# Kernel tuning notes

Hardware: AMD Instinct MI355X
Metric: run time of the kernel (lower is better)

## Reference

```python
import jax, jax.numpy as jnp
import numpy as np

B, S, H, N = 2, 2048, 1024, 16
D = H // N


def setup_inputs() -> dict:
    key = jax.random.key(0)
    k1, k2, k3 = jax.random.split(key, 3)
    # Xavier-uniform-ish init for projection weights
    lim_in = (6.0 / (H + 3 * H)) ** 0.5
    lim_out = (6.0 / (H + H)) ** 0.5
    return {
        "hidden_states": jax.random.normal(k1, (B, S, H), dtype=jnp.float32),
        "w_in": jax.random.uniform(k2, (3 * H, H), minval=-lim_in, maxval=lim_in, dtype=jnp.float32),
        "b_in": jnp.zeros((3 * H,), dtype=jnp.float32),
        "w_out": jax.random.uniform(k3, (H, H), minval=-lim_out, maxval=lim_out, dtype=jnp.float32),
        "b_out": jnp.zeros((H,), dtype=jnp.float32),
    }


def reference(hidden_states, w_in, b_in, w_out, b_out):
    b, s, h = hidden_states.shape
    qkv = hidden_states @ w_in.T + b_in  # [B,S,3H]
    q, k, v = jnp.split(qkv, 3, axis=-1)
    # [B,S,H] -> [B,N,S,D]
    def to_heads(x):
        return x.reshape(b, s, N, D).transpose(0, 2, 1, 3)
    q, k, v = to_heads(q), to_heads(k), to_heads(v)
    scale = D ** -0.5
    scores = jnp.einsum("bnqd,bnkd->bnqk", q, k) * scale  # [B,N,S,S]
    causal = jnp.triu(jnp.ones((s, s), dtype=bool), k=1)
    scores = jnp.where(causal, -jnp.inf, scores)
    attn = jax.nn.softmax(scores, axis=-1)
    out = jnp.einsum("bnqk,bnkd->bnqd", attn, v)  # [B,N,S,D]
    out = out.transpose(0, 2, 1, 3).reshape(b, s, h)
    return out @ w_out.T + b_out
```

## Files before the change

### kernel.cpp

```cpp
#include <hip/hip_runtime.h>
#include <hip/hip_bf16.h>

#define BB 2
#define SS 2048
#define HH 1024
#define NH 16
#define DD 64
#define H3 3072
#define MM (BB*SS)

typedef unsigned short u16;
typedef unsigned int u32;
typedef __attribute__((ext_vector_type(8))) short bf16x8;
typedef __attribute__((ext_vector_type(4))) float f32x4;

__device__ __forceinline__ u16 f2bf(float f) {
    union { float f; u32 u; } v; v.f = f;
    u32 u = v.u;
    u += 0x7fffu + ((u >> 16) & 1u);
    return (u16)(u >> 16);
}
__device__ __forceinline__ float bf2f(u16 h) {
    union { u32 u; float f; } v; v.u = ((u32)h) << 16;
    return v.f;
}
__device__ __forceinline__ u32 pack2bf(float a, float b) {
    __hip_bfloat162 h = __float22bfloat162_rn(float2{a, b});
    u32 u; __builtin_memcpy(&u, &h, 4);
    return u;
}
__device__ __forceinline__ float exp2v(float x) {
    float r;
    asm volatile("v_exp_f32 %0, %1" : "=v"(r) : "v"(x));
    return r;
}
__device__ __forceinline__ void gl_lds16(const void* g, void* l) {
    __builtin_amdgcn_global_load_lds(
        (const __attribute__((address_space(1))) u32*)g,
        (__attribute__((address_space(3))) u32*)l, 16, 0, 0);
}
__device__ __forceinline__ int ginv(int R) {
    return (R & 35) | ((R & 8) << 1) | ((R & 4) << 1) | ((R & 16) >> 2);
}

__global__ void cvt3bf(const float4* __restrict__ s0, uint2* __restrict__ d0, int n0,
                       const float4* __restrict__ s1, uint2* __restrict__ d1, int n1,
                       const float4* __restrict__ s2, uint2* __restrict__ d2, int n2) {
    int i = blockIdx.x * blockDim.x + threadIdx.x;
    const int tot = n0 + n1 + n2;
    for (; i < tot; i += gridDim.x * blockDim.x) {
        const float4* s; uint2* d; int j;
        if (i < n0)            { s = s0; d = d0; j = i; }
        else if (i < n0 + n1)  { s = s1; d = d1; j = i - n0; }
        else                   { s = s2; d = d2; j = i - n0 - n1; }
        float4 v = s[j];
        uint2 o; o.x = pack2bf(v.x, v.y); o.y = pack2bf(v.z, v.w);
        d[j] = o;
    }
}

template<int BN, int MODE>
__global__ __launch_bounds__(256, 3)
void gemm_k2(const u16* __restrict__ A, const u16* __restrict__ Bbf,
             const u16* __restrict__ biasbf, void* __restrict__ Cptr,
             u16* __restrict__ Qo, u16* __restrict__ Ko, u16* __restrict__ Vto,
             int M, int Nn, int K)
{
    constexpr int NFR = BN / 32;
    __shared__ __align__(16) u16 Alds[2][128 * 32];
    __shared__ __align__(16) u16 Blds[2][BN * 32];
    const int tid = threadIdx.x;
    const int w = tid >> 6, lane = tid & 63, quad = lane >> 4, l16 = lane & 15;
    const int gx = gridDim.x, nwg = gx * gridDim.y;
    const int f = blockIdx.y * gx + blockIdx.x;
    const int wg = (f & 7) * (nwg >> 3) + (f >> 3);
    const int m0 = (wg % gx) * 128, n0 = (wg / gx) * BN;
    const int wm = w >> 1, wn = w & 1;
    const int rA4 = lane >> 2, c8b = (lane & 3) * 8;

    f32x4 acc[4][NFR] = {};

#define GSTAGE(k0_, bi_) do {                                                  \
    _Pragma("unroll")                                                          \
    for (int q = 0; q < 2; ++q) {                                              \
        int row0 = w * 32 + q * 16;                                            \
        gl_lds16(&A[(size_t)(m0 + row0 + rA4) * K + (k0_) + c8b],              \
                 &Alds[bi_][row0 * 32]);                                       \
    }                                                                          \
    _Pragma("unroll")                                                          \
    for (int q = 0; q < BN / 64; ++q) {                                        \
        int row0 = w * (BN / 4) + q * 16;                                      \
        gl_lds16(&Bbf[(size_t)(n0 + row0 + rA4) * K + (k0_) + c8b],            \
                 &Blds[bi_][row0 * 32]);                                       \
    }                                                                          \
} while (0)

    const int NT = K >> 5;
    GSTAGE(0, 0);
    for (int t = 0; t < NT; ++t) {
        const int cur = t & 1;
        __syncthreads();
        if (t + 1 < NT) GSTAGE((t + 1) << 5, cur ^ 1);

        bf16x8 af[4], bfr[NFR];
#pragma unroll
        for (int mi = 0; mi < 4; ++mi)
            af[mi] = *(const bf16x8*)&Alds[cur][(wm * 64 + mi * 16 + l16) * 32 + quad * 8];
#pragma unroll
        for (int ni = 0; ni < NFR; ++ni)
            bfr[ni] = *(const bf16x8*)&Blds[cur][(wn * (BN / 2) + ni * 16 + l16) * 32 + quad * 8];
#pragma unroll
        for (int mi = 0; mi < 4; ++mi)
#pragma unroll
            for (int ni = 0; ni < NFR; ++ni)
                acc[mi][ni] = __builtin_amdgcn_mfma_f32_16x16x32_bf16(
                    af[mi], bfr[ni], acc[mi][ni], 0, 0, 0);
    }
#undef GSTAGE

#pragma unroll
    for (int mi = 0; mi < 4; ++mi) {
        int row_b = m0 + wm * 64 + mi * 16 + quad * 4;
#pragma unroll
        for (int ni = 0; ni < NFR; ++ni) {
            int col = n0 + wn * (BN / 2) + ni * 16 + l16;
            float bv = bf2f(biasbf[col]);
            if constexpr (MODE == 1) {
#pragma unroll
                for (int i = 0; i < 4; ++i)
                    ((float*)Cptr)[(size_t)(row_b + i) * Nn + col] = acc[mi][ni][i] + bv;
            } else {
                if (col < 1024) {
#pragma unroll
                    for (int i = 0; i < 4; ++i)
                        Qo[(size_t)(row_b + i) * 1024 + col] =
                            f2bf((acc[mi][ni][i] + bv) * 0.18033688f);
                } else if (col < 2048) {
#pragma unroll
                    for (int i = 0; i < 4; ++i)
                        Ko[(size_t)(row_b + i) * 1024 + (col - 1024)] =
                            f2bf(acc[mi][ni][i] + bv);
                } else {
                    int d = col - 2048, hh = d >> 6, dd = d & 63;
                    int b = row_b >> 11, s = row_b & 2047;
                    u16 t0 = f2bf(acc[mi][ni][0] + bv), t1 = f2bf(acc[mi][ni][1] + bv);
                    u16 t2 = f2bf(acc[mi][ni][2] + bv), t3 = f2bf(acc[mi][ni][3] + bv);
                    uint2 pk; pk.x = (u32)t0 | ((u32)t1 << 16);
                    pk.y = (u32)t2 | ((u32)t3 << 16);
                    *(uint2*)&Vto[((size_t)((b * 16 + hh) * 64 + dd)) * 2048 + s] = pk;
                }
            }
        }
    }
}

__global__ __launch_bounds__(256, 2)
void attn_v10(const u16* __restrict__ Q, const u16* __restrict__ Kb,
              const u16* __restrict__ Vt, u16* __restrict__ attn_out) {
    const int bid = blockIdx.x;
    const int r8 = bid & 7, qq = bid >> 3;
    const int pr = qq >> 2, g = (qq & 3) * 8 + r8;
    const int h = g & 15, b = g >> 4;
    const int tid = threadIdx.x;
    const int w = tid >> 6, lane = tid & 63, quad = lane >> 4, l16 = lane & 15;
    __shared__ __align__(16) u16 Klds[2][64 * 64];
    __shared__ __align__(16) u16 Vlds[2][64 * 64];

    const int sl = lane >> 3, cch = lane & 7;
    const int rho0 = (2 * w) * 8 + sl, rho1 = (2 * w + 1) * 8 + sl;
    const int gcs = (cch ^ sl) * 8;
    const int kg0 = ginv(rho0), kg1 = ginv(rho1);
    const int ls0 = (2 * w) * 512, ls1 = (2 * w + 1) * 512;
    const int xk0 = (quad ^ (l16 & 7)) * 8;
    const int xk1 = ((quad + 4) ^ (l16 & 7)) * 8;

    for (int half = 0; half < 2; ++half) {
        const int qt = half ? pr : (31 - pr);
        const int q0 = qt * 64;
        const int T = qt + 1;

        const u16* Qb = Q  + (size_t)(b * SS + q0) * 1024 + h * 64;
        const u16* Kg = Kb + (size_t)(b * SS) * 1024 + h * 64;
        const u16* Vg = Vt + (size_t)((b * 16 + h) * 64) * 2048;

#define STAGE_T(kv0_, bi_) do {                                               \
        gl_lds16(&Kg[(size_t)((kv0_) + kg0) * 1024 + gcs], &Klds[bi_][ls0]);  \
        gl_lds16(&Kg[(size_t)((kv0_) + kg1) * 1024 + gcs], &Klds[bi_][ls1]);  \
        gl_lds16(&Vg[(size_t)rho0 * 2048 + (kv0_) + gcs], &Vlds[bi_][ls0]);   \
        gl_lds16(&Vg[(size_t)rho1 * 2048 + (kv0_) + gcs], &Vlds[bi_][ls1]);   \
    } while (0)

        bf16x8 qf0 = *(const bf16x8*)&Qb[(size_t)(w * 16 + l16) * 1024 + quad * 8];
        bf16x8 qf1 = *(const bf16x8*)&Qb[(size_t)(w * 16 + l16) * 1024 + 32 + quad * 8];

        f32x4 oacc[4] = {};
        float lp = 0.f;

        __syncthreads();
        STAGE_T(0, 0);

        for (int t = 0; t < T; ++t) {
            const int cur = t & 1;
            __syncthreads();
            if (t + 1 < T) STAGE_T((t + 1) * 64, cur ^ 1);
            const u16* Kc = Klds[cur];
            const u16* Vc = Vlds[cur];
            f32x4 sacc[4] = {};
#pragma unroll
            for (int ni = 0; ni < 4; ++ni) {
                const int rb = (ni * 16 + l16) * 64;
                bf16x8 kf0 = *(const bf16x8*)&Kc[rb + xk0];
                bf16x8 kf1 = *(const bf16x8*)&Kc[rb + xk1];
                sacc[ni] = __builtin_amdgcn_mfma_f32_16x16x32_bf16(kf0, qf0, sacc[ni], 0, 0, 0);
                sacc[ni] = __builtin_amdgcn_mfma_f32_16x16x32_bf16(kf1, qf1, sacc[ni], 0, 0, 0);
            }
            u32 pk[4][2];
            if (t + 1 < T) {
#pragma unroll
                for (int ni = 0; ni < 4; ++ni) {
                    float p0 = exp2v(sacc[ni][0]), p1 = exp2v(sacc[ni][1]);
                    float p2 = exp2v(sacc[ni][2]), p3 = exp2v(sacc[ni][3]);
                    lp += (p0 + p1) + (p2 + p3);
                    pk[ni][0] = pack2bf(p0, p1);
                    pk[ni][1] = pack2bf(p2, p3);
                }
            } else {
                const int thr = w * 16 + l16;
#pragma unroll
                for (int ni = 0; ni < 4; ++ni) {
                    const int pb = 32 * (ni >> 1) + 8 * quad + 4 * (ni & 1);
                    float pv[4];
#pragma unroll
                    for (int i = 0; i < 4; ++i) {
                        float e = exp2v(sacc[ni][i]);
                        pv[i] = (pb + i <= thr) ? e : 0.f;
                    }
                    lp += (pv[0] + pv[1]) + (pv[2] + pv[3]);
                    pk[ni][0] = pack2bf(pv[0], pv[1]);
                    pk[ni][1] = pack2bf(pv[2], pv[3]);
                }
            }
            union { u32 u[4]; bf16x8 v; } pf0, pf1;
            pf0.u[0] = pk[0][0]; pf0.u[1] = pk[0][1];
            pf0.u[2] = pk[1][0]; pf0.u[3] = pk[1][1];
            pf1.u[0] = pk[2][0]; pf1.u[1] = pk[2][1];
            pf1.u[2] = pk[3][0]; pf1.u[3] = pk[3][1];
#pragma unroll
            for (int ni = 0; ni < 4; ++ni) {
                const int rb = (ni * 16 + l16) * 64;
                bf16x8 vf0 = *(const bf16x8*)&Vc[rb + xk0];
                bf16x8 vf1 = *(const bf16x8*)&Vc[rb + xk1];
                oacc[ni] = __builtin_amdgcn_mfma_f32_16x16x32_bf16(pf0.v, vf0, oacc[ni], 0, 0, 0);
                oacc[ni] = __builtin_amdgcn_mfma_f32_16x16x32_bf16(pf1.v, vf1, oacc[ni], 0, 0, 0);
            }
        }

        lp += __shfl_xor(lp, 16, 64);
        lp += __shfl_xor(lp, 32, 64);
        float linv[4];
#pragma unroll
        for (int i = 0; i < 4; ++i)
            linv[i] = 1.0f / __shfl(lp, quad * 4 + i, 64);

        u16* ob = attn_out + (size_t)(b * SS + q0 + w * 16) * 1024 + h * 64;
#pragma unroll
        for (int ni = 0; ni < 4; ++ni)
#pragma unroll
            for (int i = 0; i < 4; ++i)
                ob[(size_t)(quad * 4 + i) * 1024 + ni * 16 + l16] =
                    f2bf(oacc[ni][i] * linv[i]);
#undef STAGE_T
    }
}

extern "C" void kernel_launch(void* const* d_in, const int* in_sizes, int n_in,
                              void* d_out, int out_size, void* d_ws, size_t ws_size,
                              hipStream_t stream) {
    const float* hidden = (const float*)d_in[0];
    const float* w_in   = (const float*)d_in[1];
    const float* b_in   = (const float*)d_in[2];
    const float* w_out  = (const float*)d_in[3];
    const float* b_out  = (const float*)d_in[4];
    float* out = (float*)d_out;

    char* ws = (char*)d_ws;
    u16* hid_bf  = (u16*)d_out;
    u16* wi_bf   = (u16*)ws;
    u16* bi_bf   = (u16*)(ws + 6291456);
    u16* attn_ws = (u16*)ws;
    u16* Qbuf    = (u16*)(ws + 8388608);
    u16* wo_bf   = (u16*)(ws + 8388608);
    u16* bo_bf   = (u16*)(ws + 8388608 + 2097152);
    u16* Kbuf    = (u16*)(ws + 16777216);
    u16* Vtbuf   = (u16*)(ws + 25165824);

    cvt3bf<<<dim3(2048), dim3(256), 0, stream>>>(
        (const float4*)hidden, (uint2*)hid_bf, 1048576,
        (const float4*)w_in,   (uint2*)wi_bf,  786432,
        (const float4*)b_in,   (uint2*)bi_bf,  768);
    gemm_k2<128, 2><<<dim3(32, 24), dim3(256), 0, stream>>>(
        hid_bf, wi_bf, bi_bf, nullptr, Qbuf, Kbuf, Vtbuf, MM, H3, HH);
    attn_v10<<<dim3(512), dim3(256), 0, stream>>>(
        Qbuf, Kbuf, Vtbuf, attn_ws);
    cvt3bf<<<dim3(512), dim3(256), 0, stream>>>(
        (const float4*)w_out, (uint2*)wo_bf, 262144,
        (const float4*)b_out, (uint2*)bo_bf, 256,
        nullptr, nullptr, 0);
    gemm_k2<64, 1><<<dim3(32, 16), dim3(256), 0, stream>>>(
        attn_ws, wo_bf, bo_bf, out, nullptr, nullptr, nullptr, MM, HH, HH);
}
```

Before: 176.4 us.

## Replace QKV projection GEMM with 256x256-tile 8-wave pipelined kernel

Swaps the 128x128-tile QKV GEMM for a new 512-thread kernel that computes 256x256 output tiles. It uses a 128 KB LDS double buffer with XOR-swizzled layout and direct global-to-LDS loads, interleaved with MFMA quarter-phases through explicit vmcnt waits, barriers and setprio. The larger tiles raise data reuse, and the fine-grained staging aims to hide load latency behind MFMA work. In exchange the grid shrinks to 192 blocks, so fewer workgroups are in flight. The hand-tuned wait counts are fragile and must exactly match the number of outstanding loads.

```diff
diff --git a/kernel.cpp b/kernel.cpp
--- a/kernel.cpp
+++ b/kernel.cpp
@@ -42,6 +42,8 @@
 __device__ __forceinline__ int ginv(int R) {
     return (R & 35) | ((R & 8) << 1) | ((R & 4) << 1) | ((R & 16) >> 2);
 }
+
+#define VMW(N) asm volatile("s_waitcnt vmcnt(" #N ")" ::: "memory")
 
 __global__ void cvt3bf(const float4* __restrict__ s0, uint2* __restrict__ d0, int n0,
                        const float4* __restrict__ s1, uint2* __restrict__ d1, int n1,
@@ -56,6 +58,126 @@
         float4 v = s[j];
         uint2 o; o.x = pack2bf(v.x, v.y); o.y = pack2bf(v.z, v.w);
         d[j] = o;
+    }
+}
+
+__global__ __launch_bounds__(512, 2)
+void gemm8_qkv(const u16* __restrict__ Aw, const u16* __restrict__ Bw,
+               const u16* __restrict__ biasbf,
+               u16* __restrict__ Qo, u16* __restrict__ Ko, u16* __restrict__ Vto)
+{
+    __shared__ __align__(16) u16 L[65536];
+    const int tid = threadIdx.x;
+    const int w = tid >> 6, lane = tid & 63, quad = lane >> 4, l16 = lane & 15;
+    const int wm = w >> 2, wn = w & 3;
+    const int f = blockIdx.x;
+    const int wgs = (f & 7) * 24 + (f >> 3);
+    const int m0 = (wgs & 15) * 256, n0 = (wgs >> 4) * 256;
+    const int rl8 = lane >> 3;
+    const int gcs = ((lane & 7) ^ rl8) * 8;
+    const int xk0 = (quad ^ (l16 & 7)) * 8;
+    const int xk1 = ((quad + 4) ^ (l16 & 7)) * 8;
+
+    f32x4 acc[8][4] = {};
+
+#define STAGE8(ISB, H_, BUF, KT) do {                                          \
+    const u16* gsrc_ = (ISB) ? Bw : Aw;                                        \
+    const int gr0_ = ((ISB) ? n0 : m0) + (H_) * 128;                           \
+    _Pragma("unroll")                                                          \
+    for (int j = 0; j < 2; ++j) {                                              \
+        int s_ = 2 * w + j;                                                    \
+        gl_lds16(&gsrc_[(size_t)(gr0_ + s_ * 8 + rl8) * 1024 + (KT) * 64 + gcs], \
+                 &L[((BUF) * 4 + (ISB) * 2 + (H_)) * 8192 + s_ * 512]);        \
+    }                                                                          \
+} while (0)
+
+#define PH(MH, NH, CBUF, STG, WT) do {                                         \
+    bf16x8 afr[4][2], bfr2[2][2];                                              \
+    const u16* Ab_ = &L[((CBUF) * 4 + (MH)) * 8192];                           \
+    const u16* Bb_ = &L[((CBUF) * 4 + 2 + (NH)) * 8192];                       \
+    _Pragma("unroll")                                                          \
+    for (int m4 = 0; m4 < 4; ++m4) {                                           \
+        int r_ = (((((MH) * 4 + m4) * 2 + wm) & 7) << 4) + l16;                \
+        afr[m4][0] = *(const bf16x8*)&Ab_[r_ * 64 + xk0];                      \
+        afr[m4][1] = *(const bf16x8*)&Ab_[r_ * 64 + xk1];                      \
+    }                                                                          \
+    _Pragma("unroll")                                                          \
+    for (int n2 = 0; n2 < 2; ++n2) {                                           \
+        int rb_ = (((((NH) * 2 + n2) * 4 + wn) & 7) << 4) + l16;               \
+        bfr2[n2][0] = *(const bf16x8*)&Bb_[rb_ * 64 + xk0];                    \
+        bfr2[n2][1] = *(const bf16x8*)&Bb_[rb_ * 64 + xk1];                    \
+    }                                                                          \
+    STG;                                                                       \
+    __builtin_amdgcn_s_barrier();                                              \
+    __builtin_amdgcn_s_setprio(1);                                             \
+    _Pragma("unroll")                                                          \
+    for (int m4 = 0; m4 < 4; ++m4)                                             \
+        _Pragma("unroll")                                                      \
+        for (int n2 = 0; n2 < 2; ++n2) {                                       \
+            acc[(MH)*4+m4][(NH)*2+n2] = __builtin_amdgcn_mfma_f32_16x16x32_bf16( \
+                afr[m4][0], bfr2[n2][0], acc[(MH)*4+m4][(NH)*2+n2], 0, 0, 0);  \
+            acc[(MH)*4+m4][(NH)*2+n2] = __builtin_amdgcn_mfma_f32_16x16x32_bf16( \
+                afr[m4][1], bfr2[n2][1], acc[(MH)*4+m4][(NH)*2+n2], 0, 0, 0);  \
+        }                                                                      \
+    __builtin_amdgcn_s_setprio(0);                                             \
+    WT;                                                                        \
+    __builtin_amdgcn_s_barrier();                                              \
+} while (0)
+
+    STAGE8(0, 0, 0, 0); STAGE8(1, 0, 0, 0);
+    STAGE8(0, 1, 0, 0); STAGE8(1, 1, 0, 0);
+    STAGE8(0, 0, 1, 1); STAGE8(1, 0, 1, 1);
+    VMW(8);
+    __builtin_amdgcn_s_barrier();
+
+    for (int it = 0; it < 7; ++it) {
+        PH(0, 0, 0, STAGE8(0, 1, 1, 2 * it + 1), VMW(6));
+        PH(0, 1, 0, STAGE8(1, 1, 1, 2 * it + 1), VMW(10));
+        PH(1, 0, 0, STAGE8(0, 0, 0, 2 * it + 2), ((void)0));
+        PH(1, 1, 0, STAGE8(1, 0, 0, 2 * it + 2), VMW(8));
+        PH(0, 0, 1, STAGE8(0, 1, 0, 2 * it + 2), VMW(6));
+        PH(0, 1, 1, STAGE8(1, 1, 0, 2 * it + 2), VMW(10));
+        PH(1, 0, 1, STAGE8(0, 0, 1, 2 * it + 3), ((void)0));
+        PH(1, 1, 1, STAGE8(1, 0, 1, 2 * it + 3), VMW(8));
+    }
+    PH(0, 0, 0, STAGE8(0, 1, 1, 15), VMW(6));
+    PH(0, 1, 0, STAGE8(1, 1, 1, 15), VMW(10));
+    PH(1, 0, 0, ((void)0), ((void)0));
+    PH(1, 1, 0, ((void)0), VMW(4));
+    PH(0, 0, 1, ((void)0), VMW(0));
+    PH(0, 1, 1, ((void)0), ((void)0));
+    PH(1, 0, 1, ((void)0), ((void)0));
+    PH(1, 1, 1, ((void)0), ((void)0));
+#undef PH
+#undef STAGE8
+
+#pragma unroll
+    for (int mi = 0; mi < 8; ++mi) {
+        int row_b = m0 + (2 * mi + wm) * 16 + quad * 4;
+#pragma unroll
+        for (int ni = 0; ni < 4; ++ni) {
+            int col = n0 + (4 * ni + wn) * 16 + l16;
+            float bv = bf2f(biasbf[col]);
+            if (col < 1024) {
+#pragma unroll
+                for (int i = 0; i < 4; ++i)
+                    Qo[(size_t)(row_b + i) * 1024 + col] =
+                        f2bf((acc[mi][ni][i] + bv) * 0.18033688f);
+            } else if (col < 2048) {
+#pragma unroll
+                for (int i = 0; i < 4; ++i)
+                    Ko[(size_t)(row_b + i) * 1024 + (col - 1024)] =
+                        f2bf(acc[mi][ni][i] + bv);
+            } else {
+                int d = col - 2048, hh = d >> 6, dd = d & 63;
+                int b = row_b >> 11, s = row_b & 2047;
+                u16 t0 = f2bf(acc[mi][ni][0] + bv), t1 = f2bf(acc[mi][ni][1] + bv);
+                u16 t2 = f2bf(acc[mi][ni][2] + bv), t3 = f2bf(acc[mi][ni][3] + bv);
+                uint2 pk; pk.x = (u32)t0 | ((u32)t1 << 16);
+                pk.y = (u32)t2 | ((u32)t3 << 16);
+                *(uint2*)&Vto[((size_t)((b * 16 + hh) * 64 + dd)) * 2048 + s] = pk;
+            }
+        }
     }
 }
 
@@ -129,26 +251,6 @@
 #pragma unroll
                 for (int i = 0; i < 4; ++i)
                     ((float*)Cptr)[(size_t)(row_b + i) * Nn + col] = acc[mi][ni][i] + bv;
-            } else {
-                if (col < 1024) {
-#pragma unroll
-                    for (int i = 0; i < 4; ++i)
-                        Qo[(size_t)(row_b + i) * 1024 + col] =
-                            f2bf((acc[mi][ni][i] + bv) * 0.18033688f);
-                } else if (col < 2048) {
-#pragma unroll
-                    for (int i = 0; i < 4; ++i)
-                        Ko[(size_t)(row_b + i) * 1024 + (col - 1024)] =
-                            f2bf(acc[mi][ni][i] + bv);
-                } else {
-                    int d = col - 2048, hh = d >> 6, dd = d & 63;
-                    int b = row_b >> 11, s = row_b & 2047;
-                    u16 t0 = f2bf(acc[mi][ni][0] + bv), t1 = f2bf(acc[mi][ni][1] + bv);
-                    u16 t2 = f2bf(acc[mi][ni][2] + bv), t3 = f2bf(acc[mi][ni][3] + bv);
-                    uint2 pk; pk.x = (u32)t0 | ((u32)t1 << 16);
-                    pk.y = (u32)t2 | ((u32)t3 << 16);
-                    *(uint2*)&Vto[((size_t)((b * 16 + hh) * 64 + dd)) * 2048 + s] = pk;
-                }
             }
         }
     }
@@ -298,8 +400,8 @@
         (const float4*)hidden, (uint2*)hid_bf, 1048576,
         (const float4*)w_in,   (uint2*)wi_bf,  786432,
         (const float4*)b_in,   (uint2*)bi_bf,  768);
-    gemm_k2<128, 2><<<dim3(32, 24), dim3(256), 0, stream>>>(
-        hid_bf, wi_bf, bi_bf, nullptr, Qbuf, Kbuf, Vtbuf, MM, H3, HH);
+    gemm8_qkv<<<dim3(192), dim3(512), 0, stream>>>(
+        hid_bf, wi_bf, bi_bf, Qbuf, Kbuf, Vtbuf);
     attn_v10<<<dim3(512), dim3(256), 0, stream>>>(
         Qbuf, Kbuf, Vtbuf, attn_ws);
     cvt3bf<<<dim3(512), dim3(256), 0, stream>>>(
```

New measurement: 181.8 us. +3.1%, slower.
